# Performance work log

Measured on AMD Instinct MI355X. Metric: run time of the kernel, lower is better.

## Reference

```python
import jax, jax.numpy as jnp
import numpy as np

MARGIN = 0.5


def setup_inputs() -> dict:
    key = jax.random.key(0)
    k1, k2, k3 = jax.random.split(key, 3)
    B, D = 8192, 128
    anchor = jax.random.normal(k1, (B, D), dtype=jnp.float32)
    positive = jax.random.normal(k2, (B, D), dtype=jnp.float32)
    labels = jax.random.randint(k3, (B,), 0, 100, dtype=jnp.int64)
    return {"anchor": anchor, "positive": positive, "labels": labels}


def _l2_normalize(x, eps=1e-12):
    # matches F.normalize(p=2, dim=1): x / max(||x||, eps)
    n = jnp.sqrt(jnp.sum(x * x, axis=1, keepdims=True))
    return x / jnp.maximum(n, eps)


def reference(anchor, positive, labels):
    a = _l2_normalize(anchor)   # [B, D]
    p = _l2_normalize(positive)  # [B, D]

    # pairwise euclidean distances among normalized anchors:
    # ||a_i - a_j||^2 = 2 - 2 a_i . a_j  (unit vectors)
    gram = jnp.einsum('id,jd->ij', a, a)              # [B, B]
    dist = jnp.sqrt(jnp.maximum(2.0 - 2.0 * gram, 0.0))

    # mask out same-label pairs (includes diagonal)
    same = labels[None, :] == labels[:, None]
    dist = jnp.where(same, jnp.inf, dist)

    min_dist = jnp.min(dist, axis=1)                  # [B]
    neg_dist = min_dist * min_dist                    # squared distance to hard negative

    pos_dist = jnp.sum((a - p) ** 2, axis=1)          # [B]

    loss = jax.nn.relu(pos_dist - neg_dist + MARGIN)
    return jnp.mean(loss)
```

## Files before the change

### kernel.cpp

```cpp
#include <hip/hip_runtime.h>
#include <stdint.h>

#define NROWS 8192
#define DIM 128

typedef __bf16 bf16x8 __attribute__((ext_vector_type(8)));
typedef float floatx4 __attribute__((ext_vector_type(4)));

static __device__ __forceinline__ unsigned short f2bf(float f) {
    unsigned int u = __float_as_uint(f);
    unsigned int r = (u + 0x7FFFu + ((u >> 16) & 1u)) >> 16;
    return (unsigned short)r;
}

static __device__ __forceinline__ int swz(int g) {
    return (g & ~15) | ((g & 15) ^ ((g >> 4) & 7));
}

__global__ __launch_bounds__(256) void normalize_kernel(
    const float* __restrict__ anchor, const float* __restrict__ positive,
    unsigned short* __restrict__ a_hat, float* __restrict__ pos_ws,
    int* __restrict__ g_ws)
{
    const int wave = threadIdx.x >> 6;
    const int lane = threadIdx.x & 63;
    const int row  = blockIdx.x * 4 + wave;

    const float2* arow = (const float2*)(anchor   + row * DIM);
    const float2* prow = (const float2*)(positive + row * DIM);
    float2 a = arow[lane];
    float2 p = prow[lane];

    float sa  = a.x * a.x + a.y * a.y;
    float sp  = p.x * p.x + p.y * p.y;
    float sap = a.x * p.x + a.y * p.y;
    #pragma unroll
    for (int off = 32; off; off >>= 1) {
        sa  += __shfl_xor(sa,  off);
        sp  += __shfl_xor(sp,  off);
        sap += __shfl_xor(sap, off);
    }
    float na  = fmaxf(sqrtf(sa), 1e-12f);
    float npn = fmaxf(sqrtf(sp), 1e-12f);
    float inv = 1.0f / na;

    ushort2 pack;
    pack.x = f2bf(a.x * inv);
    pack.y = f2bf(a.y * inv);
    ((ushort2*)a_hat)[row * 64 + lane] = pack;

    if (lane == 0) {
        pos_ws[row] = 2.0f - 2.0f * sap / (na * npn);
        g_ws[row]   = 0x3F800000;
    }
}

__global__ __launch_bounds__(256, 4) void gram_kernel(
    const unsigned short* __restrict__ a_hat, const int* __restrict__ labels,
    int* __restrict__ g_ws)
{
    const int tid  = threadIdx.x;
    const int lane = tid & 63;
    const int wave = tid >> 6;
    const int quad = lane >> 4;
    const int l15  = lane & 15;

    const int rowBlock = blockIdx.x >> 4;
    const int nchunk   = blockIdx.x & 15;
    const int rowBase  = rowBlock * 128 + wave * 32;

    const uint4* A = (const uint4*)a_hat;

    __shared__ uint4 smem[2][512];

    bf16x8 afrag[2][4];
    #pragma unroll
    for (int s = 0; s < 2; ++s) {
        int r = rowBase + s * 16 + l15;
        #pragma unroll
        for (int k = 0; k < 4; ++k) {
            uint4 v = A[r * 16 + k * 4 + quad];
            afrag[s][k] = __builtin_bit_cast(bf16x8, v);
        }
    }

    int rlab[2][4];
    #pragma unroll
    for (int s = 0; s < 2; ++s)
        #pragma unroll
        for (int e = 0; e < 4; ++e)
            rlab[s][e] = labels[rowBase + s * 16 + quad * 4 + e];

    float gmax[2][4];
    #pragma unroll
    for (int s = 0; s < 2; ++s)
        #pragma unroll
        for (int e = 0; e < 4; ++e)
            gmax[s][e] = -4.0f;

    const int colBase = nchunk * 512;
    const uint4* Gp = A + colBase * 16;

    uint4 p0 = Gp[tid];
    uint4 p1 = Gp[tid + 256];
    smem[0][swz(tid)]       = p0;
    smem[0][swz(tid + 256)] = p1;
    __syncthreads();

    for (int cb = 0; cb < 16; ++cb) {
        const int cur = cb & 1;

        if (cb < 15) {
            p0 = Gp[(cb + 1) * 512 + tid];
            p1 = Gp[(cb + 1) * 512 + tid + 256];
        }

        const int C = colBase + cb * 32;
        int clab0 = labels[C + l15];
        int clab1 = labels[C + 16 + l15];

        bf16x8 bfrag[2][4];
        #pragma unroll
        for (int ns = 0; ns < 2; ++ns) {
            int c = ns * 16 + l15;
            #pragma unroll
            for (int k = 0; k < 4; ++k) {
                int g = c * 16 + k * 4 + quad;
                bfrag[ns][k] = __builtin_bit_cast(bf16x8, smem[cur][swz(g)]);
            }
        }

        #pragma unroll
        for (int ms = 0; ms < 2; ++ms) {
            #pragma unroll
            for (int ns = 0; ns < 2; ++ns) {
                floatx4 acc = {0.f, 0.f, 0.f, 0.f};
                #pragma unroll
                for (int k = 0; k < 4; ++k)
                    acc = __builtin_amdgcn_mfma_f32_16x16x32_bf16(
                              afrag[ms][k], bfrag[ns][k], acc, 0, 0, 0);
                const int cl = ns ? clab1 : clab0;
                #pragma unroll
                for (int e = 0; e < 4; ++e) {
                    float v = (cl != rlab[ms][e]) ? acc[e] : -4.0f;
                    gmax[ms][e] = fmaxf(gmax[ms][e], v);
                }
            }
        }

        if (cb < 15) {
            smem[cur ^ 1][swz(tid)]       = p0;
            smem[cur ^ 1][swz(tid + 256)] = p1;
            __syncthreads();
        }
    }

    #pragma unroll
    for (int s = 0; s < 2; ++s) {
        #pragma unroll
        for (int e = 0; e < 4; ++e) {
            float v = gmax[s][e];
            #pragma unroll
            for (int off = 1; off < 16; off <<= 1)
                v = fmaxf(v, __shfl_xor(v, off));
            if (l15 == 0) {
                int r = rowBase + s * 16 + quad * 4 + e;
                atomicMax(g_ws + r, __float_as_int(2.0f + v));
            }
        }
    }
}

__global__ __launch_bounds__(256) void loss_kernel(
    const float* __restrict__ pos_ws, const int* __restrict__ g_ws,
    float* __restrict__ out)
{
    const int i = blockIdx.x * 256 + threadIdx.x;
    float g    = __int_as_float(g_ws[i]) - 2.0f;
    float neg  = fmaxf(2.0f - 2.0f * g, 0.0f);
    float loss = fmaxf(pos_ws[i] - neg + 0.5f, 0.0f);

    #pragma unroll
    for (int off = 32; off; off >>= 1)
        loss += __shfl_xor(loss, off);

    __shared__ float ws[4];
    if ((threadIdx.x & 63) == 0) ws[threadIdx.x >> 6] = loss;
    __syncthreads();
    if (threadIdx.x == 0) {
        float s = ws[0] + ws[1] + ws[2] + ws[3];
        atomicAdd(out, s * (1.0f / 8192.0f));
    }
}

extern "C" void kernel_launch(void* const* d_in, const int* in_sizes, int n_in,
                              void* d_out, int out_size, void* d_ws, size_t ws_size,
                              hipStream_t stream) {
    const float* anchor   = (const float*)d_in[0];
    const float* positive = (const float*)d_in[1];
    const int*   labels   = (const int*)d_in[2];
    float* out = (float*)d_out;

    char* ws = (char*)d_ws;
    unsigned short* a_hat  = (unsigned short*)ws;
    float*          pos_ws = (float*)(ws + 2 * 1024 * 1024);
    int*            g_ws   = (int*)  (ws + 2 * 1024 * 1024 + 32 * 1024);

    hipMemsetAsync(d_out, 0, sizeof(float), stream);
    normalize_kernel<<<NROWS / 4, 256, 0, stream>>>(anchor, positive, a_hat, pos_ws, g_ws);
    gram_kernel<<<1024, 256, 0, stream>>>(a_hat, labels, g_ws);
    loss_kernel<<<NROWS / 256, 256, 0, stream>>>(pos_ws, g_ws, out);
}
```

Before: 90.27 us.

## Exploit Gram matrix symmetry with triangular tiling and row-plus-column max updates

The Gram kernel now covers only the upper-triangular set of 256-row by 128-column tiles. It maps each block to a tile with a closed-form sqrt index inversion. Each tile updates the row maxima through global atomics and the column maxima through a shared-memory atomicMax buffer that is later flushed to global memory, which roughly halves the MFMA work. The output memset is folded into the normalize kernel, removing one launch. In exchange there are more atomics per tile, the double-buffered loop is dropped in favour of one up-front column load, and occupancy falls to 3 blocks per CU to make room for the larger register tile.

```diff
diff --git a/kernel.cpp b/kernel.cpp
--- a/kernel.cpp
+++ b/kernel.cpp
@@ -20,8 +20,10 @@
 __global__ __launch_bounds__(256) void normalize_kernel(
     const float* __restrict__ anchor, const float* __restrict__ positive,
     unsigned short* __restrict__ a_hat, float* __restrict__ pos_ws,
-    int* __restrict__ g_ws)
+    int* __restrict__ g_ws, float* __restrict__ out)
 {
+    if (blockIdx.x == 0 && threadIdx.x == 0) *out = 0.0f;
+
     const int wave = threadIdx.x >> 6;
     const int lane = threadIdx.x & 63;
     const int row  = blockIdx.x * 4 + wave;
@@ -55,7 +57,7 @@
     }
 }
 
-__global__ __launch_bounds__(256, 4) void gram_kernel(
+__global__ __launch_bounds__(256, 3) void gram_kernel(
     const unsigned short* __restrict__ a_hat, const int* __restrict__ labels,
     int* __restrict__ g_ws)
 {
@@ -65,110 +67,114 @@
     const int quad = lane >> 4;
     const int l15  = lane & 15;
 
-    const int rowBlock = blockIdx.x >> 4;
-    const int nchunk   = blockIdx.x & 15;
-    const int rowBase  = rowBlock * 128 + wave * 32;
+    const int bid = blockIdx.x;
+    int rb = (int)((65.0f - sqrtf(4225.0f - 4.0f * (float)bid)) * 0.5f);
+    while (rb * (65 - rb) > bid) --rb;
+    while ((rb + 1) * (64 - rb) <= bid) ++rb;
+    const int cc = bid - rb * (65 - rb) + 2 * rb;
+
+    const int rowBase = rb * 256 + wave * 64;
+    const int colBase = cc * 128;
 
     const uint4* A = (const uint4*)a_hat;
 
-    __shared__ uint4 smem[2][512];
-
-    bf16x8 afrag[2][4];
-    #pragma unroll
-    for (int s = 0; s < 2; ++s) {
-        int r = rowBase + s * 16 + l15;
-        #pragma unroll
-        for (int k = 0; k < 4; ++k) {
-            uint4 v = A[r * 16 + k * 4 + quad];
-            afrag[s][k] = __builtin_bit_cast(bf16x8, v);
-        }
-    }
-
-    int rlab[2][4];
-    #pragma unroll
-    for (int s = 0; s < 2; ++s)
+    __shared__ uint4 smem[2048];
+    __shared__ int   colmax[128];
+
+    uint4 st[8];
+    #pragma unroll
+    for (int i = 0; i < 8; ++i)
+        st[i] = A[colBase * 16 + i * 256 + tid];
+
+    if (tid < 128) colmax[tid] = (int)0x80000000;
+
+    bf16x8 afrag[4][4];
+    #pragma unroll
+    for (int ms = 0; ms < 4; ++ms) {
+        const int r = rowBase + ms * 16 + l15;
+        #pragma unroll
+        for (int k = 0; k < 4; ++k)
+            afrag[ms][k] = __builtin_bit_cast(bf16x8, A[r * 16 + k * 4 + quad]);
+    }
+
+    int4 rlab[4];
+    #pragma unroll
+    for (int ms = 0; ms < 4; ++ms)
+        rlab[ms] = *(const int4*)(labels + rowBase + ms * 16 + quad * 4);
+
+    #pragma unroll
+    for (int i = 0; i < 8; ++i)
+        smem[swz(i * 256 + tid)] = st[i];
+    __syncthreads();
+
+    float gmax[4][4];
+    #pragma unroll
+    for (int ms = 0; ms < 4; ++ms)
         #pragma unroll
         for (int e = 0; e < 4; ++e)
-            rlab[s][e] = labels[rowBase + s * 16 + quad * 4 + e];
-
-    float gmax[2][4];
-    #pragma unroll
-    for (int s = 0; s < 2; ++s)
-        #pragma unroll
-        for (int e = 0; e < 4; ++e)
-            gmax[s][e] = -4.0f;
-
-    const int colBase = nchunk * 512;
-    const uint4* Gp = A + colBase * 16;
-
-    uint4 p0 = Gp[tid];
-    uint4 p1 = Gp[tid + 256];
-    smem[0][swz(tid)]       = p0;
-    smem[0][swz(tid + 256)] = p1;
-    __syncthreads();
-
-    for (int cb = 0; cb < 16; ++cb) {
-        const int cur = cb & 1;
-
-        if (cb < 15) {
-            p0 = Gp[(cb + 1) * 512 + tid];
-            p1 = Gp[(cb + 1) * 512 + tid + 256];
-        }
-
+            gmax[ms][e] = -4.0f;
+
+    #pragma unroll
+    for (int cb = 0; cb < 4; ++cb) {
         const int C = colBase + cb * 32;
-        int clab0 = labels[C + l15];
-        int clab1 = labels[C + 16 + l15];
+        const int clab0 = labels[C + l15];
+        const int clab1 = labels[C + 16 + l15];
 
         bf16x8 bfrag[2][4];
         #pragma unroll
         for (int ns = 0; ns < 2; ++ns) {
-            int c = ns * 16 + l15;
+            const int c = ns * 16 + l15;
             #pragma unroll
             for (int k = 0; k < 4; ++k) {
-                int g = c * 16 + k * 4 + quad;
-                bfrag[ns][k] = __builtin_bit_cast(bf16x8, smem[cur][swz(g)]);
+                const int g = cb * 512 + c * 16 + k * 4 + quad;
+                bfrag[ns][k] = __builtin_bit_cast(bf16x8, smem[swz(g)]);
             }
         }
 
         #pragma unroll
-        for (int ms = 0; ms < 2; ++ms) {
+        for (int ns = 0; ns < 2; ++ns) {
+            const int cl = ns ? clab1 : clab0;
+            float cmax = -4.0f;
             #pragma unroll
-            for (int ns = 0; ns < 2; ++ns) {
+            for (int ms = 0; ms < 4; ++ms) {
                 floatx4 acc = {0.f, 0.f, 0.f, 0.f};
                 #pragma unroll
                 for (int k = 0; k < 4; ++k)
                     acc = __builtin_amdgcn_mfma_f32_16x16x32_bf16(
                               afrag[ms][k], bfrag[ns][k], acc, 0, 0, 0);
-                const int cl = ns ? clab1 : clab0;
                 #pragma unroll
                 for (int e = 0; e < 4; ++e) {
-                    float v = (cl != rlab[ms][e]) ? acc[e] : -4.0f;
+                    const int rle = (e == 0) ? rlab[ms].x : (e == 1) ? rlab[ms].y
+                                  : (e == 2) ? rlab[ms].z : rlab[ms].w;
+                    float v = (cl != rle) ? acc[e] : -4.0f;
                     gmax[ms][e] = fmaxf(gmax[ms][e], v);
+                    cmax        = fmaxf(cmax, v);
                 }
             }
+            cmax = fmaxf(cmax, __shfl_xor(cmax, 16));
+            cmax = fmaxf(cmax, __shfl_xor(cmax, 32));
+            if (quad == 0)
+                atomicMax(&colmax[cb * 32 + ns * 16 + l15],
+                          __float_as_int(2.0f + cmax));
         }
-
-        if (cb < 15) {
-            smem[cur ^ 1][swz(tid)]       = p0;
-            smem[cur ^ 1][swz(tid + 256)] = p1;
-            __syncthreads();
-        }
-    }
-
-    #pragma unroll
-    for (int s = 0; s < 2; ++s) {
+    }
+
+    #pragma unroll
+    for (int ms = 0; ms < 4; ++ms) {
         #pragma unroll
         for (int e = 0; e < 4; ++e) {
-            float v = gmax[s][e];
+            float v = gmax[ms][e];
             #pragma unroll
             for (int off = 1; off < 16; off <<= 1)
                 v = fmaxf(v, __shfl_xor(v, off));
-            if (l15 == 0) {
-                int r = rowBase + s * 16 + quad * 4 + e;
-                atomicMax(g_ws + r, __float_as_int(2.0f + v));
-            }
+            if (l15 == 0)
+                atomicMax(g_ws + rowBase + ms * 16 + quad * 4 + e,
+                          __float_as_int(2.0f + v));
         }
     }
+
+    __syncthreads();
+    if (tid < 128) atomicMax(g_ws + colBase + tid, colmax[tid]);
 }
 
 __global__ __launch_bounds__(256) void loss_kernel(
@@ -206,8 +212,7 @@
     float*          pos_ws = (float*)(ws + 2 * 1024 * 1024);
     int*            g_ws   = (int*)  (ws + 2 * 1024 * 1024 + 32 * 1024);
 
-    hipMemsetAsync(d_out, 0, sizeof(float), stream);
-    normalize_kernel<<<NROWS / 4, 256, 0, stream>>>(anchor, positive, a_hat, pos_ws, g_ws);
-    gram_kernel<<<1024, 256, 0, stream>>>(a_hat, labels, g_ws);
+    normalize_kernel<<<NROWS / 4, 256, 0, stream>>>(anchor, positive, a_hat, pos_ws, g_ws, out);
+    gram_kernel<<<1056, 256, 0, stream>>>(a_hat, labels, g_ws);
     loss_kernel<<<NROWS / 256, 256, 0, stream>>>(pos_ws, g_ws, out);
 }
```

New measurement: 115.8 us. 1.28x slower.
